# Kernel optimization log

Hardware: AMD Instinct MI355X
Metric: run time of the kernel (lower is better)

## Reference

```python
import jax, jax.numpy as jnp
import numpy as np

B, M, NT, V, D, H, E, S = 4, 12, 12, 10000, 64, 3, 512, 32


def setup_inputs() -> dict:
    key = jax.random.key(0)
    ks = jax.random.split(key, 16)
    def rn(k, shape, scale=0.05):
        return jax.random.normal(k, shape, dtype=jnp.float32) * scale
    return {
        "tendency": jax.random.normal(ks[0], (B, M, V), dtype=jnp.float32),
        "periodicity": jax.random.normal(ks[1], (B, NT, V), dtype=jnp.float32),
        "edges": jax.random.randint(ks[2], (H, E, S), 0, V),
        "w1": rn(ks[3], (1, D)), "b1": rn(ks[4], (D,)),
        "w2": rn(ks[5], (D, D)), "b2": rn(ks[6], (D,)),
        "attn_w": rn(ks[7], (D, D)), "attn_a": rn(ks[8], (2 * D, 1)),
        "w_ih": rn(ks[9], (4 * D, D)), "w_hh": rn(ks[10], (4 * D, D)),
        "b_ih": rn(ks[11], (4 * D,)), "b_hh": rn(ks[12], (4 * D,)),
        "w_out": rn(ks[13], (2 * D, 1)), "b_out": rn(ks[14], (1,)),
    }


def _hypersage(X, edges, w, b):
    # X: (N, V, F); edges: (E, S) node indices. All edges have size S <= Q,
    # so torch's random subsampling is the identity.
    n, v, f = X.shape
    e, s = edges.shape
    gathered = X[:, edges, :]                      # (N, E, S, F)
    agg = gathered.mean(axis=2)                    # (N, E, F)
    flat = edges.reshape(-1)                       # (E*S,)
    contrib = jnp.broadcast_to(agg[:, :, None, :], (n, e, s, f)).reshape(n, e * s, f)
    X_out = jnp.zeros((n, v, f), X.dtype).at[:, flat, :].add(contrib)
    deg = jnp.zeros((v,), X.dtype).at[flat].add(1.0)
    deg = jnp.maximum(deg, 1.0)
    X_out = X_out / deg[None, :, None]
    return X_out @ w + b                           # Linear fc


def _attention(Xs, attn_w, attn_a):
    # Xs: (H, N, V, D)
    ref = Xs.mean(axis=0)                          # (N, V, D)
    wx = Xs @ attn_w                               # (H, N, V, D)
    wr = ref @ attn_w                              # (N, V, D)
    z = jnp.concatenate([wx, jnp.broadcast_to(wr[None], wx.shape)], axis=-1) @ attn_a
    z = jax.nn.leaky_relu(z, negative_slope=0.2)   # (H, N, V, 1)
    alpha = jax.nn.softmax(z, axis=0)
    return (alpha * Xs).sum(axis=0)                # (N, V, D)


def _lstm_final(x, w_ih, w_hh, b_ih, b_hh):
    # x: (BV, T, D) -> final hidden state (BV, D). PyTorch gate order i,f,g,o.
    bv, t, d = x.shape
    xg = x @ w_ih.T + (b_ih + b_hh)                # precompute input gates (BV, T, 4D)
    def step(carry, xg_t):
        h, c = carry
        g = xg_t + h @ w_hh.T
        i, f, gg, o = jnp.split(g, 4, axis=-1)
        c = jax.nn.sigmoid(f) * c + jax.nn.sigmoid(i) * jnp.tanh(gg)
        h = jax.nn.sigmoid(o) * jnp.tanh(c)
        return (h, c), None
    h0 = jnp.zeros((bv, d), x.dtype)
    (h, _), _ = jax.lax.scan(step, (h0, h0), jnp.swapaxes(xg, 0, 1))
    return h


def _branch(seq, edges, w1, b1, w2, b2, attn_w, attn_a, w_ih, w_hh, b_ih, b_hh):
    b, t, v = seq.shape
    X = seq.reshape(b * t, v, 1)                   # fold time into batch (same DAMHG per step)
    def per_hg(e):
        return _hypersage(_hypersage(X, e, w1, b1), e, w2, b2)
    xs = jax.vmap(per_hg)(edges)                   # (H, B*T, V, D)
    fused = _attention(xs, attn_w, attn_a)         # (B*T, V, D)
    d = fused.shape[-1]
    seq_v = fused.reshape(b, t, v, d).transpose(0, 2, 1, 3).reshape(b * v, t, d)
    h = _lstm_final(seq_v, w_ih, w_hh, b_ih, b_hh)
    return h.reshape(b, v, d)


def reference(tendency, periodicity, edges, w1, b1, w2, b2, attn_w, attn_a, w_ih, w_hh, b_ih, b_hh, w_out, b_out):
    h_t = _branch(tendency, edges, w1, b1, w2, b2, attn_w, attn_a, w_ih, w_hh, b_ih, b_hh)
    h_p = _branch(periodicity, edges, w1, b1, w2, b2, attn_w, attn_a, w_ih, w_hh, b_ih, b_hh)
    fusion = jnp.concatenate([h_t, h_p], axis=-1)  # (B, V, 2D)
    out = fusion @ w_out + b_out                   # (B, V, 1)
    return out[..., 0]
```

## Files before the change

### kernel.cpp

```cpp
#include <hip/hip_runtime.h>

#define NV 10000
#define NB 4
#define NTT 12
#define NSEQ 48
#define NH 3
#define NE 512
#define NS 32
#define ND 64
#define NVT 313

#define S_U   0
#define S_C1  64
#define S_V1  128
#define S_V2  192
#define S_SC  256
#define S_GU  272
#define S_GC  528
#define S_G0  784
#define F_INV 1040
#define F_M   (F_INV + NH*NV)
#define F_PQ  (F_M + NH*NV)
#define F_HT  (F_PQ + 4*NV*NSEQ)
#define I_CNT (F_HT + 2*NB*NV)
#define I_CUR (I_CNT + NH*NV)
#define I_OFF (I_CUR + NH*NV)
#define I_SLOT (I_OFF + NH*NV)
#define F_DYN (I_SLOT + NH*NE*NS)
#define XT_SZ  (NV*NSEQ)
#define AGG_SZ (NH*NE*NSEQ)
#define YZ_SZ  (NH*NV*NSEQ)

#define NZERO (2*NH*NV + NB*NV)
#define ZBLK  ((NZERO + 255) / 256)
#define TRB   ((NV + 127) / 128)

#define L2E 1.442695040888963f

typedef __attribute__((ext_vector_type(8))) _Float16 f16x8;
typedef __attribute__((ext_vector_type(4))) float f32x4;

__device__ __forceinline__ unsigned short f2h(float x) {
  union { _Float16 h; unsigned short u; } c;
  c.h = (_Float16)x;
  return c.u;
}
__device__ __forceinline__ f16x8 ldsH(const unsigned short* p) {
  union { uint4 u; f16x8 v; } x;
  x.u = *(const uint4*)p;
  return x.v;
}

__global__ void k_init(const float* __restrict__ w1, const float* __restrict__ b1,
                       const float* __restrict__ w2, const float* __restrict__ b2,
                       const float* __restrict__ attn_w, const float* __restrict__ attn_a,
                       const float* __restrict__ w_ih, const float* __restrict__ b_ih,
                       const float* __restrict__ b_hh, float* __restrict__ ws,
                       int* __restrict__ cnt, float* __restrict__ out,
                       const float* __restrict__ s0, const float* __restrict__ s1,
                       float* __restrict__ xT, int xtS) {
  const int tid = threadIdx.x;
  if (blockIdx.x > ZBLK) {
    __shared__ float tile[128][49];
    const int bx = blockIdx.x - 1 - ZBLK;
    const int brn = bx / TRB;
    const int v0 = (bx % TRB) * 128;
    const float* seq = brn ? s1 : s0;
    float* o = xT + (size_t)brn * xtS;
    for (int i = tid; i < 128 * NSEQ; i += 256) {
      const int n = i / 128, vl = i % 128;
      const int v = v0 + vl;
      tile[vl][n] = (v < NV) ? seq[n * NV + v] : 0.0f;
    }
    __syncthreads();
    for (int i = tid; i < 128 * NSEQ; i += 256) {
      const int vl = i / NSEQ, n = i % NSEQ;
      const int v = v0 + vl;
      if (v < NV) o[v * NSEQ + n] = tile[vl][n];
    }
    return;
  }
  if (blockIdx.x != 0) {
    const int g = (blockIdx.x - 1) * 256 + tid;
    if (g < 2 * NH * NV) cnt[g] = 0;
    else if (g < NZERO) out[g - 2 * NH * NV] = 0.0f;
    return;
  }
  __shared__ float u_s[64], c1_s[64];
  if (tid < 64) {
    float v1 = 0.f, v2 = 0.f, u = 0.f, c1 = 0.f;
    for (int d = 0; d < 64; ++d) {
      const float aw = attn_w[tid * 64 + d];
      v1 += aw * attn_a[d];
      v2 += aw * attn_a[64 + d];
      const float w2v = w2[d * 64 + tid];
      u  += w1[d] * w2v;
      c1 += b1[d] * w2v;
    }
    ws[S_U + tid] = u;  ws[S_C1 + tid] = c1;
    ws[S_V1 + tid] = v1; ws[S_V2 + tid] = v2;
    u_s[tid] = u; c1_s[tid] = c1;
  }
  __syncthreads();
  if (tid == 0) {
    float al = 0.f, be = 0.f, ga = 0.f, de = 0.f, ep = 0.f;
    for (int d = 0; d < 64; ++d) {
      const float v1 = ws[S_V1 + d], v2 = ws[S_V2 + d];
      al += u_s[d] * v1;  be += c1_s[d] * v1;
      ga += u_s[d] * v2;  de += c1_s[d] * v2;
      ep += b2[d] * (v1 + v2);
    }
    ws[S_SC + 0] = al; ws[S_SC + 1] = be; ws[S_SC + 2] = ga;
    ws[S_SC + 3] = de; ws[S_SC + 4] = ep;
  }
  {
    const int j = tid;
    float gu = 0.f, gc = 0.f, g0 = 0.f;
    for (int d = 0; d < 64; ++d) {
      const float w = w_ih[j * 64 + d];
      gu += w * u_s[d]; gc += w * c1_s[d]; g0 += w * b2[d];
    }
    ws[S_GU + j] = gu; ws[S_GC + j] = gc;
    ws[S_G0 + j] = g0 + b_ih[j] + b_hh[j];
  }
}

__global__ void k_count(const int* __restrict__ edges, int* __restrict__ counts) {
  const int g = blockIdx.x * 256 + threadIdx.x;
  if (g >= NH * NE * NS) return;
  const int h = g >> 14;
  atomicAdd(&counts[h * NV + edges[g]], 1);
}

__global__ void k_scan(const int* __restrict__ counts, int* __restrict__ offs,
                       float* __restrict__ invdeg, float* __restrict__ mvec) {
  const int h = blockIdx.x;
  const int tid = threadIdx.x;
  const int base = h * NV;
  const int CH = 10;
  int local[10];
  int run = 0;
  for (int i = 0; i < CH; ++i) {
    const int v = tid * CH + i;
    const int c = (v < NV) ? counts[base + v] : 0;
    local[i] = run; run += c;
  }
  __shared__ int sd[1024];
  sd[tid] = run;
  __syncthreads();
  int acc = run;
  for (int off = 1; off < 1024; off <<= 1) {
    const int t = (tid >= off) ? sd[tid - off] : 0;
    __syncthreads();
    acc += t; sd[tid] = acc;
    __syncthreads();
  }
  const int excl = acc - run;
  for (int i = 0; i < CH; ++i) {
    const int v = tid * CH + i;
    if (v < NV) {
      offs[base + v] = excl + local[i];
      const int c = counts[base + v];
      invdeg[base + v] = 1.0f / (float)((c > 0) ? c : 1);
      mvec[base + v] = (c > 0) ? 1.0f : 0.0f;
    }
  }
}

__global__ void k_fe1(const int* __restrict__ edges, const int* __restrict__ offs,
                      int* __restrict__ cursor, int* __restrict__ slot_edge,
                      const float* __restrict__ xT, int xtS,
                      float* __restrict__ agg, int aggS) {
  const int tid = threadIdx.x;
  if (blockIdx.x < 192) {
    const int g = blockIdx.x * 256 + tid;
    const int h = g >> 14;
    const int e = (g >> 5) & (NE - 1);
    const int v = edges[g];
    const int pos = atomicAdd(&cursor[h * NV + v], 1);
    slot_edge[h * NE * NS + offs[h * NV + v] + pos] = e;
    return;
  }
  const int job = blockIdx.x - 192;
  const int brn = job / 576;
  const int g = (job % 576) * 256 + tid;
  const float* x = xT + (size_t)brn * xtS;
  float* a = agg + (size_t)brn * aggS;
  const int sub = g & 7;
  const int o = g >> 3;
  const int n0 = (o % 12) * 4;
  const int e = (o / 12) % NE;
  const int h = o / (12 * NE);
  const int* ep = edges + (h * NE + e) * NS + sub * 4;
  float4 acc = make_float4(0.f, 0.f, 0.f, 0.f);
  #pragma unroll
  for (int s = 0; s < 4; ++s) {
    const float4 t = *(const float4*)&x[ep[s] * NSEQ + n0];
    acc.x += t.x; acc.y += t.y; acc.z += t.z; acc.w += t.w;
  }
  #pragma unroll
  for (int m = 1; m < 8; m <<= 1) {
    acc.x += __shfl_xor(acc.x, m);
    acc.y += __shfl_xor(acc.y, m);
    acc.z += __shfl_xor(acc.z, m);
    acc.w += __shfl_xor(acc.w, m);
  }
  if (sub == 0) {
    acc.x *= (1.0f / NS); acc.y *= (1.0f / NS); acc.z *= (1.0f / NS); acc.w *= (1.0f / NS);
    *(float4*)&a[(h * NE + e) * NSEQ + n0] = acc;
  }
}

__global__ void k_fill(const int* __restrict__ edges, const int* __restrict__ offs,
                       int* __restrict__ cursor, int* __restrict__ slot_edge) {
  const int g = blockIdx.x * 256 + threadIdx.x;
  if (g >= NH * NE * NS) return;
  const int h = g >> 14;
  const int e = (g >> 5) & (NE - 1);
  const int v = edges[g];
  const int pos = atomicAdd(&cursor[h * NV + v], 1);
  slot_edge[h * NE * NS + offs[h * NV + v] + pos] = e;
}

__global__ void k_eagg1(const int* __restrict__ edges, const float* __restrict__ xT,
                        int xtS, float* __restrict__ agg, int aggS) {
  const int g = blockIdx.x * 256 + threadIdx.x;
  if (g >= NH * NE * 12 * 8) return;
  const float* x = xT + (size_t)blockIdx.y * xtS;
  float* a = agg + (size_t)blockIdx.y * aggS;
  const int sub = g & 7;
  const int o = g >> 3;
  const int n0 = (o % 12) * 4;
  const int e = (o / 12) % NE;
  const int h = o / (12 * NE);
  const int* ep = edges + (h * NE + e) * NS + sub * 4;
  float4 acc = make_float4(0.f, 0.f, 0.f, 0.f);
  #pragma unroll
  for (int s = 0; s < 4; ++s) {
    const float4 t = *(const float4*)&x[ep[s] * NSEQ + n0];
    acc.x += t.x; acc.y += t.y; acc.z += t.z; acc.w += t.w;
  }
  #pragma unroll
  for (int m = 1; m < 8; m <<= 1) {
    acc.x += __shfl_xor(acc.x, m);
    acc.y += __shfl_xor(acc.y, m);
    acc.z += __shfl_xor(acc.z, m);
    acc.w += __shfl_xor(acc.w, m);
  }
  if (sub == 0) {
    acc.x *= (1.0f / NS); acc.y *= (1.0f / NS); acc.z *= (1.0f / NS); acc.w *= (1.0f / NS);
    *(float4*)&a[(h * NE + e) * NSEQ + n0] = acc;
  }
}

__global__ void k_eagg2(const int* __restrict__ edges, const float* __restrict__ ysum,
                        int yS, const float* __restrict__ invdeg,
                        float* __restrict__ agg, int aggS) {
  const int g = blockIdx.x * 256 + threadIdx.x;
  if (g >= NH * NE * 12 * 8) return;
  const float* y = ysum + (size_t)blockIdx.y * yS;
  float* a = agg + (size_t)blockIdx.y * aggS;
  const int sub = g & 7;
  const int o = g >> 3;
  const int n0 = (o % 12) * 4;
  const int e = (o / 12) % NE;
  const int h = o / (12 * NE);
  const int* ep = edges + (h * NE + e) * NS + sub * 4;
  float4 acc = make_float4(0.f, 0.f, 0.f, 0.f);
  #pragma unroll
  for (int s = 0; s < 4; ++s) {
    const int v = ep[s];
    const float iv = invdeg[h * NV + v];
    const float4 t = *(const float4*)&y[(h * NV + v) * NSEQ + n0];
    acc.x += t.x * iv; acc.y += t.y * iv; acc.z += t.z * iv; acc.w += t.w * iv;
  }
  #pragma unroll
  for (int m = 1; m < 8; m <<= 1) {
    acc.x += __shfl_xor(acc.x, m);
    acc.y += __shfl_xor(acc.y, m);
    acc.z += __shfl_xor(acc.z, m);
    acc.w += __shfl_xor(acc.w, m);
  }
  if (sub == 0) {
    acc.x *= (1.0f / NS); acc.y *= (1.0f / NS); acc.z *= (1.0f / NS); acc.w *= (1.0f / NS);
    *(float4*)&a[(h * NE + e) * NSEQ + n0] = acc;
  }
}

__global__ void k_vg(const int* __restrict__ counts, const int* __restrict__ offs,
                     const int* __restrict__ slot_edge, const float* __restrict__ agg,
                     int aggS, float* __restrict__ outv, int outS) {
  const int g = blockIdx.x * 256 + threadIdx.x;
  if (g >= NH * NV * 12) return;
  const float* a = agg + (size_t)blockIdx.y * aggS;
  float* o = outv + (size_t)blockIdx.y * outS;
  const int n0 = (g % 12) * 4;
  const int v = (g / 12) % NV;
  const int h = g / (12 * NV);
  const int beg = offs[h * NV + v];
  const int cnt = counts[h * NV + v];
  const int* se = slot_edge + h * NE * NS;
  float4 acc = make_float4(0.f, 0.f, 0.f, 0.f);
  for (int i = 0; i < cnt; ++i) {
    const int e = se[beg + i];
    const float4 t = *(const float4*)&a[(h * NE + e) * NSEQ + n0];
    acc.x += t.x; acc.y += t.y; acc.z += t.z; acc.w += t.w;
  }
  *(float4*)&o[(h * NV + v) * NSEQ + n0] = acc;
}

__global__ void k_vgattn(const int* __restrict__ counts, const int* __restrict__ offs,
                         const int* __restrict__ slot_edge, const float* __restrict__ agg,
                         int aggS, const float* __restrict__ invdeg,
                         const float* __restrict__ mvec, const float* __restrict__ ws,
                         unsigned int* __restrict__ pq, int br0) {
  const int g = blockIdx.x * 256 + threadIdx.x;
  if (g >= NV * 12) return;
  const int bi = blockIdx.y;
  const float* a = agg + (size_t)bi * aggS;
  unsigned int* pbuf = pq + (size_t)(bi + br0) * NV * NSEQ;
  const int n0 = (g % 12) * 4;
  const int v = g / 12;
  const float al = ws[S_SC + 0], be = ws[S_SC + 1], ga = ws[S_SC + 2],
              de = ws[S_SC + 3], ep = ws[S_SC + 4];
  union { float4 v4; float f[4]; } zh[3];
  float mh[3];
  #pragma unroll
  for (int h = 0; h < NH; ++h) {
    const int beg = offs[h * NV + v];
    const int cnt = counts[h * NV + v];
    const int* se = slot_edge + h * NE * NS;
    float4 acc = make_float4(0.f, 0.f, 0.f, 0.f);
    for (int i = 0; i < cnt; ++i) {
      const int e = se[beg + i];
      const float4 t = *(const float4*)&a[(h * NE + e) * NSEQ + n0];
      acc.x += t.x; acc.y += t.y; acc.z += t.z; acc.w += t.w;
    }
    const float iv = invdeg[h * NV + v];
    zh[h].v4 = make_float4(acc.x * iv, acc.y * iv, acc.z * iv, acc.w * iv);
    mh[h] = mvec[h * NV + v];
  }
  const float mb = (mh[0] + mh[1] + mh[2]) * (1.f / 3.f);
  uint4 o4;
  unsigned int* op = (unsigned int*)&o4;
  #pragma unroll
  for (int j = 0; j < 4; ++j) {
    const float z0 = zh[0].f[j], z1 = zh[1].f[j], z2 = zh[2].f[j];
    const float zb = (z0 + z1 + z2) * (1.f / 3.f);
    float sc[3];
    const float zt[3] = {z0, z1, z2};
    #pragma unroll
    for (int h = 0; h < NH; ++h) {
      const float s = al * zt[h] + be * mh[h] + ga * zb + de * mb + ep;
      sc[h] = (s > 0.f) ? s : 0.2f * s;
    }
    const float mx = fmaxf(sc[0], fmaxf(sc[1], sc[2]));
    const float e0 = __expf(sc[0] - mx), e1 = __expf(sc[1] - mx), e2 = __expf(sc[2] - mx);
    const float inv = 1.0f / (e0 + e1 + e2);
    const float pv = (e0 * z0 + e1 * z1 + e2 * z2) * inv;
    const float qv = (e0 * mh[0] + e1 * mh[1] + e2 * mh[2]) * inv;
    op[j] = (unsigned int)f2h(pv) | ((unsigned int)f2h(qv) << 16);
  }
  *(uint4*)&pbuf[v * NSEQ + n0] = o4;
}

#define RS2 72
__launch_bounds__(256, 4)
__global__ void k_lstm2(const float* __restrict__ w_hh, const float* __restrict__ ws,
                        const unsigned int* __restrict__ pqbase,
                        const float* __restrict__ w_out, const float* __restrict__ b_out,
                        float* __restrict__ out) {
  __shared__ __align__(16) unsigned short smem[2 * 32 * RS2];
  __shared__ unsigned int pq_sh[NTT][32];
  const int tid = threadIdx.x;
  const int w = tid >> 6, lane = tid & 63, q = lane >> 4, l15 = lane & 15;
  const int bid = blockIdx.x;
  const int vt = bid % NVT;
  const int b  = (bid / NVT) % NB;
  const int br = bid / (NVT * NB);
  const int v0 = vt * 32;
  const int d = w * 16 + l15;

  union HU { uint4 u; f16x8 v; };

  const unsigned int* pqb = pqbase + (size_t)br * NV * NSEQ;
  if (tid < 96) {
    const int s = tid / 3, f4 = tid % 3;
    const int v = v0 + s;
    uint4 val = make_uint4(0u, 0u, 0u, 0u);
    if (v < NV) val = *(const uint4*)&pqb[v * NSEQ + b * NTT + f4 * 4];
    pq_sh[f4 * 4 + 0][s] = val.x; pq_sh[f4 * 4 + 1][s] = val.y;
    pq_sh[f4 * 4 + 2][s] = val.z; pq_sh[f4 * 4 + 3][s] = val.w;
  }

  f16x8 Bf[4][2];
  #pragma unroll
  for (int g = 0; g < 4; ++g) {
    const float sc = (g == 2) ? (-2.0f * L2E) : -L2E;
    #pragma unroll
    for (int kh = 0; kh < 2; ++kh) {
      const float* wp = w_hh + (g * 64 + d) * 64 + kh * 32 + q * 8;
      const float4 lo = *(const float4*)wp;
      const float4 hi = *(const float4*)(wp + 4);
      HU f;
      f.u.x = (unsigned int)f2h(sc * lo.x) | ((unsigned int)f2h(sc * lo.y) << 16);
      f.u.y = (unsigned int)f2h(sc * lo.z) | ((unsigned int)f2h(sc * lo.w) << 16);
      f.u.z = (unsigned int)f2h(sc * hi.x) | ((unsigned int)f2h(sc * hi.y) << 16);
      f.u.w = (unsigned int)f2h(sc * hi.z) | ((unsigned int)f2h(sc * hi.w) << 16);
      Bf[g][kh] = f.v;
    }
  }

  HU bex[4];
  #pragma unroll
  for (int g = 0; g < 4; ++g) {
    const float sc = (g == 2) ? (-2.0f * L2E) : -L2E;
    const float gu = sc * ws[S_GU + g * 64 + d];
    const float gc = sc * ws[S_GC + g * 64 + d];
    const float g0 = sc * ws[S_G0 + g * 64 + d];
    bex[g].u.x = (q == 0) ? ((unsigned int)f2h(gu) | ((unsigned int)f2h(gc) << 16)) : 0u;
    bex[g].u.y = (q == 0) ? (unsigned int)f2h(g0) : 0u;
    bex[g].u.z = 0u; bex[g].u.w = 0u;
  }
  const float WO = w_out[br * 64 + d];
  const float BO = b_out[0];
  __syncthreads();

  const float K  = -2.0f * L2E;
  const float NK = 2.0f * L2E;
  f32x4 cst[2];
  float pr[2][4];
  #pragma unroll
  for (int mi = 0; mi < 2; ++mi) cst[mi] = (f32x4){0.f, 0.f, 0.f, 0.f};
  const f32x4 z4 = (f32x4){0.f, 0.f, 0.f, 0.f};

  #pragma unroll 1
  for (int t = 0; t < NTT; ++t) {
    const unsigned short* hr = smem + ((t + 1) & 1) * (32 * RS2);
    unsigned short* hw = smem + (t & 1) * (32 * RS2);
    const bool last = (t == NTT - 1);
    #pragma unroll
    for (int mi = 0; mi < 2; ++mi) {
      HU ae;
      ae.u.x = (q == 0) ? pq_sh[t][mi * 16 + l15] : 0u;
      ae.u.y = (q == 0) ? 0x3C00u : 0u;
      ae.u.z = 0u; ae.u.w = 0u;
      f32x4 aI = __builtin_amdgcn_mfma_f32_16x16x32_f16(ae.v, bex[0].v, z4, 0, 0, 0);
      f32x4 aF = __builtin_amdgcn_mfma_f32_16x16x32_f16(ae.v, bex[1].v, z4, 0, 0, 0);
      f32x4 aG = __builtin_amdgcn_mfma_f32_16x16x32_f16(ae.v, bex[2].v, z4, 0, 0, 0);
      f32x4 aO = __builtin_amdgcn_mfma_f32_16x16x32_f16(ae.v, bex[3].v, z4, 0, 0, 0);
      if (t > 0) {
        #pragma unroll
        for (int kh = 0; kh < 2; ++kh) {
          const f16x8 Ah = ldsH(&hr[(mi * 16 + l15) * RS2 + kh * 32 + q * 8]);
          aI = __builtin_amdgcn_mfma_f32_16x16x32_f16(Ah, Bf[0][kh], aI, 0, 0, 0);
          aF = __builtin_amdgcn_mfma_f32_16x16x32_f16(Ah, Bf[1][kh], aF, 0, 0, 0);
          aG = __builtin_amdgcn_mfma_f32_16x16x32_f16(Ah, Bf[2][kh], aG, 0, 0, 0);
          aO = __builtin_amdgcn_mfma_f32_16x16x32_f16(Ah, Bf[3][kh], aO, 0, 0, 0);
        }
      }
      #pragma unroll
      for (int r = 0; r < 4; ++r) {
        const float cs = cst[mi][r];
        const float ea = __builtin_amdgcn_exp2f(aI[r]);
        const float eb = __builtin_amdgcn_exp2f(aG[r]);
        const float ef = __builtin_amdgcn_exp2f(aF[r]);
        const float A  = 1.0f + ea, Bb = 1.0f + eb, Fd = 1.0f + ef;
        const float P  = A * Bb;
        const float tK = fmaf(eb, NK, K);
        const float numer = fmaf(cs, P, tK * Fd);
        const float cns = numer * __builtin_amdgcn_rcpf(Fd * P);
        cst[mi][r] = cns;
        const float ec = __builtin_amdgcn_exp2f(aO[r]);
        const float ed = __builtin_amdgcn_exp2f(cns);
        const float h = (1.0f - ed) *
            __builtin_amdgcn_rcpf((1.0f + ec) * (1.0f + ed));
        if (!last) {
          hw[(mi * 16 + q * 4 + r) * RS2 + d] = f2h(h);
        } else {
          pr[mi][r] = h * WO;
        }
      }
    }
    __syncthreads();
  }
  float* fbuf = (float*)smem;
  #pragma unroll
  for (int mi = 0; mi < 2; ++mi)
    #pragma unroll
    for (int r = 0; r < 4; ++r) {
      float v = pr[mi][r];
      v += __shfl_xor(v, 1);
      v += __shfl_xor(v, 2);
      v += __shfl_xor(v, 4);
      v += __shfl_xor(v, 8);
      if (l15 == 0) fbuf[w * 32 + mi * 16 + q * 4 + r] = v;
    }
  __syncthreads();
  if (tid < 32) {
    const int v = v0 + tid;
    if (v < NV) {
      const float s = fbuf[tid] + fbuf[32 + tid] + fbuf[64 + tid] + fbuf[96 + tid];
      atomicAdd(&out[b * NV + v], s + ((br == 0) ? BO : 0.0f));
    }
  }
}

__global__ void k_trans2(const float* __restrict__ s0, const float* __restrict__ s1,
                         float* __restrict__ xT, int xtS) {
  __shared__ float tile[128][49];
  const float* seq = blockIdx.y ? s1 : s0;
  float* o = xT + (size_t)blockIdx.y * xtS;
  const int v0 = blockIdx.x * 128;
  const int tid = threadIdx.x;
  for (int i = tid; i < 128 * NSEQ; i += 256) {
    const int n = i / 128, vl = i % 128;
    const int v = v0 + vl;
    tile[vl][n] = (v < NV) ? seq[n * NV + v] : 0.0f;
  }
  __syncthreads();
  for (int i = tid; i < 128 * NSEQ; i += 256) {
    const int vl = i / NSEQ, n = i % NSEQ;
    const int v = v0 + vl;
    if (v < NV) o[v * NSEQ + n] = tile[vl][n];
  }
}

extern "C" void kernel_launch(void* const* d_in, const int* in_sizes, int n_in,
                              void* d_out, int out_size, void* d_ws, size_t ws_size,
                              hipStream_t stream) {
  const float* tend   = (const float*)d_in[0];
  const float* peri   = (const float*)d_in[1];
  const int*   edges  = (const int*)d_in[2];
  const float* w1     = (const float*)d_in[3];
  const float* b1     = (const float*)d_in[4];
  const float* w2     = (const float*)d_in[5];
  const float* b2     = (const float*)d_in[6];
  const float* attn_w = (const float*)d_in[7];
  const float* attn_a = (const float*)d_in[8];
  const float* w_ih   = (const float*)d_in[9];
  const float* w_hh   = (const float*)d_in[10];
  const float* b_ih   = (const float*)d_in[11];
  const float* b_hh   = (const float*)d_in[12];
  const float* w_out  = (const float*)d_in[13];
  const float* b_out  = (const float*)d_in[14];
  float* out = (float*)d_out;
  float* ws  = (float*)d_ws;
  int*   iws = (int*)d_ws;
  int* cnt = iws + I_CNT;
  int* cur = iws + I_CUR;
  int* off = iws + I_OFF;
  int* sed = iws + I_SLOT;
  unsigned int* pqw = (unsigned int*)(ws + F_PQ);

  const size_t need2 = ((size_t)F_DYN + 2 * (XT_SZ + AGG_SZ + YZ_SZ)) * 4;
  const bool batched = ws_size >= need2;
  const int nb = batched ? 2 : 1;
  float* XT  = ws + F_DYN;
  float* AGG = XT + (size_t)nb * XT_SZ;
  float* YZ  = AGG + (size_t)nb * AGG_SZ;

  const int initg = batched ? (1 + ZBLK + 2 * TRB) : (1 + ZBLK);
  k_init<<<initg, 256, 0, stream>>>(
      w1, b1, w2, b2, attn_w, attn_a, w_ih, b_ih, b_hh, ws, cnt, out,
      tend, peri, XT, XT_SZ);
  k_count<<<(NH * NE * NS) / 256, 256, 0, stream>>>(edges, cnt);
  k_scan<<<NH, 1024, 0, stream>>>(cnt, off, ws + F_INV, ws + F_M);

  const int g_eagg = (NH * NE * 12 * 8) / 256;
  const int g_vg   = (NH * NV * 12 + 255) / 256;
  const int g_attn = (NV * 12 + 255) / 256;
  if (batched) {
    k_fe1<<<192 + 2 * g_eagg, 256, 0, stream>>>(edges, off, cur, sed, XT, XT_SZ, AGG, AGG_SZ);
    k_vg<<<dim3(g_vg, 2), 256, 0, stream>>>(cnt, off, sed, AGG, AGG_SZ, YZ, YZ_SZ);
    k_eagg2<<<dim3(g_eagg, 2), 256, 0, stream>>>(edges, YZ, YZ_SZ, ws + F_INV, AGG, AGG_SZ);
    k_vgattn<<<dim3(g_attn, 2), 256, 0, stream>>>(cnt, off, sed, AGG, AGG_SZ,
                                                  ws + F_INV, ws + F_M, ws, pqw, 0);
  } else {
    k_fill<<<(NH * NE * NS) / 256, 256, 0, stream>>>(edges, off, cur, sed);
    for (int br = 0; br < 2; ++br) {
      const float* seq = br ? peri : tend;
      k_trans2<<<dim3(TRB, 1), 256, 0, stream>>>(seq, seq, XT, 0);
      k_eagg1<<<dim3(g_eagg, 1), 256, 0, stream>>>(edges, XT, 0, AGG, 0);
      k_vg<<<dim3(g_vg, 1), 256, 0, stream>>>(cnt, off, sed, AGG, 0, YZ, 0);
      k_eagg2<<<dim3(g_eagg, 1), 256, 0, stream>>>(edges, YZ, 0, ws + F_INV, AGG, 0);
      k_vgattn<<<dim3(g_attn, 1), 256, 0, stream>>>(cnt, off, sed, AGG, 0,
                                                    ws + F_INV, ws + F_M, ws, pqw, br);
    }
  }
  k_lstm2<<<NVT * NB * 2, 256, 0, stream>>>(w_hh, ws, pqw, w_out, b_out, out);
}
```

Measured before the change: 223.0 us.

## Replace vertex-gather and edge-aggregate pass with precomputed edge-edge matrix GEMM

Builds a per-hypergraph edge-to-edge matrix B (NE x NE) from vertex incidence lists and inverse degrees with atomics. The second-layer edge aggregation then becomes a dense product of B with the first-layer edge aggregates, replacing the k_vg and k_eagg2 passes over all vertices. This removes one vertex-level gather pass and its intermediate traffic. In exchange it adds zeroing of a 3x512x512 buffer, an atomic-heavy build of B (quadratic in vertex degree), and a scalar-FMA GEMM.

```diff
diff --git a/kernel.cpp b/kernel.cpp
--- a/kernel.cpp
+++ b/kernel.cpp
@@ -30,6 +30,7 @@
 #define XT_SZ  (NV*NSEQ)
 #define AGG_SZ (NH*NE*NSEQ)
 #define YZ_SZ  (NH*NV*NSEQ)
+#define B_SZ   (NH*NE*NE)
 
 #define NZERO (2*NH*NV + NB*NV)
 #define ZBLK  ((NZERO + 255) / 256)
@@ -58,11 +59,12 @@
                        const float* __restrict__ b_hh, float* __restrict__ ws,
                        int* __restrict__ cnt, float* __restrict__ out,
                        const float* __restrict__ s0, const float* __restrict__ s1,
-                       float* __restrict__ xT, int xtS) {
+                       float* __restrict__ xT, int xtS,
+                       float* __restrict__ bz, int nz, int zblk) {
   const int tid = threadIdx.x;
-  if (blockIdx.x > ZBLK) {
+  if (blockIdx.x > zblk) {
     __shared__ float tile[128][49];
-    const int bx = blockIdx.x - 1 - ZBLK;
+    const int bx = blockIdx.x - 1 - zblk;
     const int brn = bx / TRB;
     const int v0 = (bx % TRB) * 128;
     const float* seq = brn ? s1 : s0;
@@ -84,6 +86,7 @@
     const int g = (blockIdx.x - 1) * 256 + tid;
     if (g < 2 * NH * NV) cnt[g] = 0;
     else if (g < NZERO) out[g - 2 * NH * NV] = 0.0f;
+    else if (g < nz) bz[g - NZERO] = 0.0f;
     return;
   }
   __shared__ float u_s[64], c1_s[64];
@@ -208,6 +211,57 @@
   if (sub == 0) {
     acc.x *= (1.0f / NS); acc.y *= (1.0f / NS); acc.z *= (1.0f / NS); acc.w *= (1.0f / NS);
     *(float4*)&a[(h * NE + e) * NSEQ + n0] = acc;
+  }
+}
+
+__global__ void k_bmat(const int* __restrict__ counts, const int* __restrict__ offs,
+                       const int* __restrict__ slot_edge, const float* __restrict__ invdeg,
+                       float* __restrict__ Bm) {
+  const int g = blockIdx.x * 256 + threadIdx.x;
+  if (g >= NH * NV) return;
+  const int c = counts[g];
+  if (c == 0) return;
+  const int h = g / NV;
+  const int beg = offs[g];
+  const int* se = slot_edge + h * NE * NS;
+  const float iv = invdeg[g];
+  for (int i = 0; i < c; ++i) {
+    float* row = Bm + ((size_t)(h * NE + se[beg + i])) * NE;
+    for (int j = 0; j < c; ++j)
+      atomicAdd(&row[se[beg + j]], iv);
+  }
+}
+
+__global__ void k_gemm(const float* __restrict__ Bm, const float* __restrict__ agg1,
+                       int aggS, float* __restrict__ agg2, int agg2S) {
+  const int g = blockIdx.x * 256 + threadIdx.x;
+  if (g >= NH * NE * 12 * 8) return;
+  const int brn = blockIdx.y;
+  const int sub = g & 7;
+  const int o = g >> 3;
+  const int n0 = (o % 12) * 4;
+  const int e = (o / 12) % NE;
+  const int h = o / (12 * NE);
+  const float* a1 = agg1 + (size_t)brn * aggS + h * NE * NSEQ;
+  const float* brow = Bm + ((size_t)(h * NE + e)) * NE + sub * 64;
+  float4 acc = make_float4(0.f, 0.f, 0.f, 0.f);
+  #pragma unroll 4
+  for (int k = 0; k < 64; ++k) {
+    const float b = brow[k];
+    const float4 t = *(const float4*)&a1[(sub * 64 + k) * NSEQ + n0];
+    acc.x = fmaf(b, t.x, acc.x); acc.y = fmaf(b, t.y, acc.y);
+    acc.z = fmaf(b, t.z, acc.z); acc.w = fmaf(b, t.w, acc.w);
+  }
+  #pragma unroll
+  for (int m = 1; m < 8; m <<= 1) {
+    acc.x += __shfl_xor(acc.x, m);
+    acc.y += __shfl_xor(acc.y, m);
+    acc.z += __shfl_xor(acc.z, m);
+    acc.w += __shfl_xor(acc.w, m);
+  }
+  if (sub == 0) {
+    acc.x *= (1.0f / NS); acc.y *= (1.0f / NS); acc.z *= (1.0f / NS); acc.w *= (1.0f / NS);
+    *(float4*)&agg2[(size_t)brn * agg2S + (h * NE + e) * NSEQ + n0] = acc;
   }
 }
 
@@ -559,24 +613,32 @@
   float* XT  = ws + F_DYN;
   float* AGG = XT + (size_t)nb * XT_SZ;
   float* YZ  = AGG + (size_t)nb * AGG_SZ;
-
-  const int initg = batched ? (1 + ZBLK + 2 * TRB) : (1 + ZBLK);
-  k_init<<<initg, 256, 0, stream>>>(
-      w1, b1, w2, b2, attn_w, attn_a, w_ih, b_ih, b_hh, ws, cnt, out,
-      tend, peri, XT, XT_SZ);
-  k_count<<<(NH * NE * NS) / 256, 256, 0, stream>>>(edges, cnt);
-  k_scan<<<NH, 1024, 0, stream>>>(cnt, off, ws + F_INV, ws + F_M);
+  float* Bm   = YZ;
+  float* AGG2 = YZ + B_SZ;
 
   const int g_eagg = (NH * NE * 12 * 8) / 256;
   const int g_vg   = (NH * NV * 12 + 255) / 256;
   const int g_attn = (NV * 12 + 255) / 256;
+
   if (batched) {
+    const int nz = NZERO + B_SZ;
+    const int zblk = (nz + 255) / 256;
+    k_init<<<1 + zblk + 2 * TRB, 256, 0, stream>>>(
+        w1, b1, w2, b2, attn_w, attn_a, w_ih, b_ih, b_hh, ws, cnt, out,
+        tend, peri, XT, XT_SZ, Bm, nz, zblk);
+    k_count<<<(NH * NE * NS) / 256, 256, 0, stream>>>(edges, cnt);
+    k_scan<<<NH, 1024, 0, stream>>>(cnt, off, ws + F_INV, ws + F_M);
     k_fe1<<<192 + 2 * g_eagg, 256, 0, stream>>>(edges, off, cur, sed, XT, XT_SZ, AGG, AGG_SZ);
-    k_vg<<<dim3(g_vg, 2), 256, 0, stream>>>(cnt, off, sed, AGG, AGG_SZ, YZ, YZ_SZ);
-    k_eagg2<<<dim3(g_eagg, 2), 256, 0, stream>>>(edges, YZ, YZ_SZ, ws + F_INV, AGG, AGG_SZ);
-    k_vgattn<<<dim3(g_attn, 2), 256, 0, stream>>>(cnt, off, sed, AGG, AGG_SZ,
+    k_bmat<<<(NH * NV + 255) / 256, 256, 0, stream>>>(cnt, off, sed, ws + F_INV, Bm);
+    k_gemm<<<dim3(g_eagg, 2), 256, 0, stream>>>(Bm, AGG, AGG_SZ, AGG2, AGG_SZ);
+    k_vgattn<<<dim3(g_attn, 2), 256, 0, stream>>>(cnt, off, sed, AGG2, AGG_SZ,
                                                   ws + F_INV, ws + F_M, ws, pqw, 0);
   } else {
+    k_init<<<1 + ZBLK, 256, 0, stream>>>(
+        w1, b1, w2, b2, attn_w, attn_a, w_ih, b_ih, b_hh, ws, cnt, out,
+        tend, peri, XT, XT_SZ, XT, NZERO, ZBLK);
+    k_count<<<(NH * NE * NS) / 256, 256, 0, stream>>>(edges, cnt);
+    k_scan<<<NH, 1024, 0, stream>>>(cnt, off, ws + F_INV, ws + F_M);
     k_fill<<<(NH * NE * NS) / 256, 256, 0, stream>>>(edges, off, cur, sed);
     for (int br = 0; br < 2; ++br) {
       const float* seq = br ? peri : tend;
```

New measurement: 290.4 us. 1.3x slower.
